# Kernel optimization log

Hardware: AMD Instinct MI355X
Metric: run time of the kernel (lower is better)

Reference implementation:

```python
import jax, jax.numpy as jnp
import numpy as np

NUM_HEADS = 8

def setup_inputs() -> dict:
    key = jax.random.key(0)
    k1, k2, k3, k4, k5 = jax.random.split(key, 5)
    B, N, C = 4, 2048, 512
    x = jax.random.normal(k1, (B, N, C), dtype=jnp.float32)
    s = 1.0 / np.sqrt(C)
    qkv_w = jax.random.uniform(k2, (3 * C, C), dtype=jnp.float32, minval=-s, maxval=s)
    qkv_b = jax.random.uniform(k3, (3 * C,), dtype=jnp.float32, minval=-s, maxval=s)
    proj_w = jax.random.uniform(k4, (C, C), dtype=jnp.float32, minval=-s, maxval=s)
    proj_b = jax.random.uniform(k5, (C,), dtype=jnp.float32, minval=-s, maxval=s)
    return {"x": x, "qkv_w": qkv_w, "qkv_b": qkv_b, "proj_w": proj_w, "proj_b": proj_b}

def reference(x, qkv_w, qkv_b, proj_w, proj_b):
    B, N, C = x.shape
    H = NUM_HEADS
    D = C // H
    scale = D ** -0.5
    # qkv: [B,N,3C] -> [3,B,H,N,D]
    qkv = (jnp.einsum('bnc,oc->bno', x, qkv_w) + qkv_b)
    qkv = qkv.reshape(B, N, 3, H, D).transpose(2, 0, 3, 1, 4)
    q, k, v = qkv[0], qkv[1], qkv[2]
    attn = jnp.einsum('bhnd,bhmd->bhnm', q, k) * scale  # [B,H,N,N]
    attn = jax.nn.softmax(attn, axis=-1)
    out = jnp.einsum('bhnm,bhmd->bhnd', attn, v)  # [B,H,N,D]
    out = out.transpose(0, 2, 1, 3).reshape(B, N, C)
    return jnp.einsum('bnc,oc->bno', out, proj_w) + proj_b
```

## Files before the change

kernel.cpp:

```cpp
#include <hip/hip_runtime.h>
#include <stdint.h>


typedef short bf16x8 __attribute__((ext_vector_type(8)));
typedef float f32x2  __attribute__((ext_vector_type(2)));
typedef float f32x4  __attribute__((ext_vector_type(4)));
typedef float f32x16 __attribute__((ext_vector_type(16)));
typedef unsigned int u32x4 __attribute__((ext_vector_type(4)));

__device__ __forceinline__ unsigned short f2bf(float f) {
    unsigned int u = __builtin_bit_cast(unsigned int, f);
    u += 0x7fffu + ((u >> 16) & 1u);
    return (unsigned short)(u >> 16);
}
__device__ __forceinline__ unsigned int pk2(float a, float b) {
    return (unsigned int)f2bf(a) | ((unsigned int)f2bf(b) << 16);
}
__device__ __forceinline__ float fexp2(float x) {
    return __builtin_amdgcn_exp2f(x);
}
__device__ __forceinline__ bf16x8 ld8_f32(const float* __restrict__ p) {
    float4 f0 = *(const float4*)p;
    float4 f1 = *(const float4*)(p + 4);
    u32x4 u = {pk2(f0.x, f0.y), pk2(f0.z, f0.w), pk2(f1.x, f1.y), pk2(f1.z, f1.w)};
    return __builtin_bit_cast(bf16x8, u);
}
__device__ __forceinline__ void async16(const void* g, void* l) {
    __builtin_amdgcn_global_load_lds(
        (const __attribute__((address_space(1))) unsigned int*)g,
        (__attribute__((address_space(3))) unsigned int*)l,
        16, 0, 0);
}

#define MFMA16(a, b, c) __builtin_amdgcn_mfma_f32_16x16x32_bf16((a), (b), (c), 0, 0, 0)
#define MFMA32(a, b, c) __builtin_amdgcn_mfma_f32_32x32x16_bf16((a), (b), (c), 0, 0, 0)

__global__ void cvt_bf16(const float* __restrict__ x,
                         const float* __restrict__ w,
                         const float* __restrict__ w2,
                         unsigned short* __restrict__ xb,
                         unsigned short* __restrict__ wb,
                         unsigned short* __restrict__ wb2)
{
    const int G = 524288 + 98304 + 32768;
    for (int idx = blockIdx.x * 256 + threadIdx.x; idx < G; idx += gridDim.x * 256) {
        if (idx < 524288)
            *(bf16x8*)(xb + (size_t)idx * 8) = ld8_f32(x + (size_t)idx * 8);
        else if (idx < 524288 + 98304) {
            int j = idx - 524288;
            *(bf16x8*)(wb + (size_t)j * 8) = ld8_f32(w + (size_t)j * 8);
        } else {
            int j = idx - 524288 - 98304;
            *(bf16x8*)(wb2 + (size_t)j * 8) = ld8_f32(w2 + (size_t)j * 8);
        }
    }
}

__global__ __launch_bounds__(256, 4)
void gemm_qkv(const unsigned short* __restrict__ A,
              const unsigned short* __restrict__ B,
              const float* __restrict__ bias,
              unsigned short* __restrict__ out0,
              unsigned short* __restrict__ out1,
              unsigned short* __restrict__ out2,
              int K)
{
    __shared__ unsigned short sA[128 * 32];
    __shared__ unsigned short sB[128 * 32];

    const int tid  = threadIdx.x;
    const int wave = tid >> 6, lane = tid & 63;
    const int l = lane & 15, q16 = lane >> 4;
    const int wm = wave >> 1, wn = wave & 1;
    const int bid = blockIdx.x;
    const int slot = bid >> 3;
    const int m0 = ((bid & 7) * 8 + slot / 12) * 128;
    const int n0 = (slot % 12) * 128;

    f32x4 acc[4][4];
#pragma unroll
    for (int i = 0; i < 4; ++i)
#pragma unroll
        for (int j = 0; j < 4; ++j)
            acc[i][j] = (f32x4){0.f, 0.f, 0.f, 0.f};

    for (int k0 = 0; k0 < K; k0 += 32) {
#pragma unroll
        for (int call = 0; call < 2; ++call) {
            int L = call * 256 + tid;
            int r = L >> 2, c = L & 3;
            async16(A + (size_t)(m0 + r) * K + k0 + c * 8, sA + L * 8);
            async16(B + (size_t)(n0 + r) * K + k0 + c * 8, sB + L * 8);
        }
        __syncthreads();

        bf16x8 af[4], bfr[4];
#pragma unroll
        for (int i = 0; i < 4; ++i)
            af[i] = *(const bf16x8*)(sA + ((wm * 64 + i * 16 + l) * 4 + q16) * 8);
#pragma unroll
        for (int j = 0; j < 4; ++j)
            bfr[j] = *(const bf16x8*)(sB + ((wn * 64 + j * 16 + l) * 4 + q16) * 8);
#pragma unroll
        for (int i = 0; i < 4; ++i)
#pragma unroll
            for (int j = 0; j < 4; ++j)
                acc[i][j] = MFMA16(af[i], bfr[j], acc[i][j]);
        __syncthreads();
    }

    const float lscale = 0.18033688f;
#pragma unroll
    for (int i = 0; i < 4; ++i) {
#pragma unroll
        for (int j = 0; j < 4; ++j) {
            int col = n0 + wn * 64 + j * 16 + l;
            float bv = bias[col];
#pragma unroll
            for (int r = 0; r < 4; ++r) {
                int row = m0 + wm * 64 + i * 16 + q16 * 4 + r;
                float val = acc[i][j][r] + bv;
                int which = col >> 9;
                int hd = (col >> 6) & 7, d = col & 63;
                int b = row >> 11, n = row & 2047;
                int bh = b * 8 + hd;
                if (which == 0) {
                    out0[(size_t)((bh * 2048) + n) * 64 + d] = f2bf(val * lscale);
                } else if (which == 1) {
                    int t = n >> 7, kh2 = (n >> 6) & 1, mt = (n >> 5) & 1;
                    int l31o = n & 31;
                    int ks = (d >> 4) & 3, h2 = (d >> 3) & 1, e = d & 7;
                    size_t frag = ((((size_t)bh * 16 + t) * 2 + kh2) * 2 + mt) * 4 + ks;
                    out1[frag * 512 + (h2 * 32 + l31o) * 8 + e] = f2bf(val);
                } else {
                    int np = (n & ~12) | ((n & 8) >> 1) | ((n & 4) << 1);
                    int t = np >> 7, kh2 = (np >> 6) & 1;
                    int c = (np >> 3) & 7, e = np & 7;
                    int m1 = (c >> 2) & 1, ks2 = (c >> 1) & 1, h2 = c & 1;
                    int dt = d >> 5, l31o = d & 31;
                    size_t frag = (((((size_t)bh * 16 + t) * 2 + kh2) * 2 + m1) * 2
                                   + ks2) * 2 + dt;
                    out2[frag * 512 + (h2 * 32 + l31o) * 8 + e] = f2bf(val);
                }
            }
        }
    }
}

__global__ __launch_bounds__(256, 4)
void gemm_out(const unsigned short* __restrict__ A,
              const unsigned short* __restrict__ B,
              const float* __restrict__ bias,
              float* __restrict__ outf,
              int K, int N)
{
    __shared__ unsigned short sA[64 * 32];
    __shared__ unsigned short sB[128 * 32];

    const int tid  = threadIdx.x;
    const int wave = tid >> 6, lane = tid & 63;
    const int l = lane & 15, q16 = lane >> 4;
    const int wm = wave >> 1, wn = wave & 1;
    const int bid = blockIdx.x;
    const int slot = bid >> 3;
    const int m0 = ((bid & 7) * 16 + (slot >> 2)) * 64;
    const int n0 = (slot & 3) * 128;

    f32x4 acc[2][4];
#pragma unroll
    for (int i = 0; i < 2; ++i)
#pragma unroll
        for (int j = 0; j < 4; ++j)
            acc[i][j] = (f32x4){0.f, 0.f, 0.f, 0.f};

    for (int k0 = 0; k0 < K; k0 += 32) {
        {
            int r = tid >> 2, c = tid & 3;
            async16(A + (size_t)(m0 + r) * K + k0 + c * 8, sA + tid * 8);
        }
#pragma unroll
        for (int call = 0; call < 2; ++call) {
            int L = call * 256 + tid;
            int r = L >> 2, c = L & 3;
            async16(B + (size_t)(n0 + r) * K + k0 + c * 8, sB + L * 8);
        }
        __syncthreads();

        bf16x8 af[2], bfr[4];
#pragma unroll
        for (int i = 0; i < 2; ++i)
            af[i] = *(const bf16x8*)(sA + ((wm * 32 + i * 16 + l) * 4 + q16) * 8);
#pragma unroll
        for (int j = 0; j < 4; ++j)
            bfr[j] = *(const bf16x8*)(sB + ((wn * 64 + j * 16 + l) * 4 + q16) * 8);
#pragma unroll
        for (int i = 0; i < 2; ++i)
#pragma unroll
            for (int j = 0; j < 4; ++j)
                acc[i][j] = MFMA16(af[i], bfr[j], acc[i][j]);
        __syncthreads();
    }

#pragma unroll
    for (int i = 0; i < 2; ++i) {
#pragma unroll
        for (int j = 0; j < 4; ++j) {
            int col = n0 + wn * 64 + j * 16 + l;
            float bv = bias[col];
#pragma unroll
            for (int r = 0; r < 4; ++r) {
                int row = m0 + wm * 32 + i * 16 + q16 * 4 + r;
                outf[(size_t)row * N + col] = acc[i][j][r] + bv;
            }
        }
    }
}

__global__ __launch_bounds__(512)
void attn_fused(const unsigned short* __restrict__ Q,
                const unsigned short* __restrict__ Kfr,
                const unsigned short* __restrict__ Vfr,
                unsigned short* __restrict__ O)
{
    __shared__ float smrg[16384 + 1024];

    const int tid  = threadIdx.x;
    const int wave = tid >> 6, lane = tid & 63;
    const int l31 = lane & 31, h = lane >> 5;
    const int qq = wave & 3, kh = wave >> 2;
    const int bid = blockIdx.x;
    const int slot = bid >> 3;
    const int bh = (bid & 7) * 4 + (slot >> 3);
    const int qc = slot & 7;
    const int q0 = qc * 256 + qq * 64;

    const unsigned short* Kb = Kfr + (size_t)bh * 131072 + kh * 4096 + lane * 8;
    const unsigned short* Vb = Vfr + (size_t)bh * 131072 + kh * 4096 + lane * 8;

    bf16x8 qf[2][4];
#pragma unroll
    for (int qt = 0; qt < 2; ++qt)
#pragma unroll
        for (int ks = 0; ks < 4; ++ks)
            qf[qt][ks] = *(const bf16x8*)(Q + (size_t)(bh * 2048 + q0 + qt * 32 + l31) * 64
                                          + ks * 16 + h * 8);

    f32x16 oacc[2][2];
#pragma unroll
    for (int qt = 0; qt < 2; ++qt)
#pragma unroll
        for (int dt = 0; dt < 2; ++dt)
#pragma unroll
            for (int e = 0; e < 16; ++e) oacc[qt][dt][e] = 0.f;
    f32x16 Zv;
#pragma unroll
    for (int e = 0; e < 16; ++e) Zv[e] = 0.f;
    f32x2 l2[2];
    l2[0] = (f32x2){0.f, 0.f};
    l2[1] = (f32x2){0.f, 0.f};

    auto softmax_pack = [&](const f32x16& s0, const f32x16& s1,
                            bf16x8& f00, bf16x8& f01,
                            bf16x8& f10, bf16x8& f11) {
        unsigned int pk0[4][2], pk1[4][2];
#pragma unroll
        for (int g = 0; g < 4; ++g) {
            float a0 = fexp2(s0[4 * g + 0]);
            float a1 = fexp2(s0[4 * g + 1]);
            float a2 = fexp2(s0[4 * g + 2]);
            float a3 = fexp2(s0[4 * g + 3]);
            l2[0] += (f32x2){a0, a1};
            l2[0] += (f32x2){a2, a3};
            pk0[g][0] = __builtin_amdgcn_perm(
                __builtin_bit_cast(unsigned int, a1),
                __builtin_bit_cast(unsigned int, a0), 0x07060302u);
            pk0[g][1] = __builtin_amdgcn_perm(
                __builtin_bit_cast(unsigned int, a3),
                __builtin_bit_cast(unsigned int, a2), 0x07060302u);
            float b0 = fexp2(s1[4 * g + 0]);
            float b1 = fexp2(s1[4 * g + 1]);
            float b2 = fexp2(s1[4 * g + 2]);
            float b3 = fexp2(s1[4 * g + 3]);
            l2[1] += (f32x2){b0, b1};
            l2[1] += (f32x2){b2, b3};
            pk1[g][0] = __builtin_amdgcn_perm(
                __builtin_bit_cast(unsigned int, b1),
                __builtin_bit_cast(unsigned int, b0), 0x07060302u);
            pk1[g][1] = __builtin_amdgcn_perm(
                __builtin_bit_cast(unsigned int, b3),
                __builtin_bit_cast(unsigned int, b2), 0x07060302u);
        }
        u32x4 bu;
        bu[0] = pk0[0][0]; bu[1] = pk0[0][1]; bu[2] = pk0[1][0]; bu[3] = pk0[1][1];
        f00 = __builtin_bit_cast(bf16x8, bu);
        bu[0] = pk0[2][0]; bu[1] = pk0[2][1]; bu[2] = pk0[3][0]; bu[3] = pk0[3][1];
        f01 = __builtin_bit_cast(bf16x8, bu);
        bu[0] = pk1[0][0]; bu[1] = pk1[0][1]; bu[2] = pk1[1][0]; bu[3] = pk1[1][1];
        f10 = __builtin_bit_cast(bf16x8, bu);
        bu[0] = pk1[2][0]; bu[1] = pk1[2][1]; bu[2] = pk1[3][0]; bu[3] = pk1[3][1];
        f11 = __builtin_bit_cast(bf16x8, bu);
    };

    bf16x8 kA[4], kB[4], vv[2][2];

#pragma unroll
    for (int ks = 0; ks < 4; ++ks)
        kA[ks] = *(const bf16x8*)(Kb + ks * 512);

    for (int t = 0; t < 16; ++t) {
        const size_t tb = (size_t)t * 8192;

#pragma unroll
        for (int ks2 = 0; ks2 < 2; ++ks2)
#pragma unroll
            for (int dt = 0; dt < 2; ++dt)
                vv[ks2][dt] = *(const bf16x8*)(Vb + tb + ks2 * 1024 + dt * 512);
#pragma unroll
        for (int ks = 0; ks < 4; ++ks)
            kB[ks] = *(const bf16x8*)(Kb + tb + 2048 + ks * 512);

        f32x16 s0, s1;
        __builtin_amdgcn_s_setprio(1);
        s0 = MFMA32(kA[0], qf[0][0], Zv);
        s1 = MFMA32(kA[0], qf[1][0], Zv);
#pragma unroll
        for (int ks = 1; ks < 4; ++ks) {
            s0 = MFMA32(kA[ks], qf[0][ks], s0);
            s1 = MFMA32(kA[ks], qf[1][ks], s1);
        }
        __builtin_amdgcn_s_setprio(0);
        {
            bf16x8 f00, f01, f10, f11;
            softmax_pack(s0, s1, f00, f01, f10, f11);
            __builtin_amdgcn_s_setprio(1);
            oacc[0][0] = MFMA32(vv[0][0], f00, oacc[0][0]);
            oacc[1][0] = MFMA32(vv[0][0], f10, oacc[1][0]);
            oacc[0][1] = MFMA32(vv[0][1], f00, oacc[0][1]);
            oacc[1][1] = MFMA32(vv[0][1], f10, oacc[1][1]);
            oacc[0][0] = MFMA32(vv[1][0], f01, oacc[0][0]);
            oacc[1][0] = MFMA32(vv[1][0], f11, oacc[1][0]);
            oacc[0][1] = MFMA32(vv[1][1], f01, oacc[0][1]);
            oacc[1][1] = MFMA32(vv[1][1], f11, oacc[1][1]);
            __builtin_amdgcn_s_setprio(0);
        }

#pragma unroll
        for (int ks2 = 0; ks2 < 2; ++ks2)
#pragma unroll
            for (int dt = 0; dt < 2; ++dt)
                vv[ks2][dt] = *(const bf16x8*)(Vb + tb + 2048 + ks2 * 1024 + dt * 512);
        if (t < 15) {
#pragma unroll
            for (int ks = 0; ks < 4; ++ks)
                kA[ks] = *(const bf16x8*)(Kb + tb + 8192 + ks * 512);
        }

        __builtin_amdgcn_s_setprio(1);
        s0 = MFMA32(kB[0], qf[0][0], Zv);
        s1 = MFMA32(kB[0], qf[1][0], Zv);
#pragma unroll
        for (int ks = 1; ks < 4; ++ks) {
            s0 = MFMA32(kB[ks], qf[0][ks], s0);
            s1 = MFMA32(kB[ks], qf[1][ks], s1);
        }
        __builtin_amdgcn_s_setprio(0);
        {
            bf16x8 f00, f01, f10, f11;
            softmax_pack(s0, s1, f00, f01, f10, f11);
            __builtin_amdgcn_s_setprio(1);
            oacc[0][0] = MFMA32(vv[0][0], f00, oacc[0][0]);
            oacc[1][0] = MFMA32(vv[0][0], f10, oacc[1][0]);
            oacc[0][1] = MFMA32(vv[0][1], f00, oacc[0][1]);
            oacc[1][1] = MFMA32(vv[0][1], f10, oacc[1][1]);
            oacc[0][0] = MFMA32(vv[1][0], f01, oacc[0][0]);
            oacc[1][0] = MFMA32(vv[1][0], f11, oacc[1][0]);
            oacc[0][1] = MFMA32(vv[1][1], f01, oacc[0][1]);
            oacc[1][1] = MFMA32(vv[1][1], f11, oacc[1][1]);
            __builtin_amdgcn_s_setprio(0);
        }
    }

    __syncthreads();
    float* sf = smrg;
    float* sl = smrg + 16384;
    if (kh == 1) {
        const int base = (qq * 64 + lane) * 64;
#pragma unroll
        for (int qt = 0; qt < 2; ++qt)
#pragma unroll
            for (int dt = 0; dt < 2; ++dt) {
                int chunk = (qt * 2 + dt) ^ (lane & 3);
                *(f32x16*)(sf + base + chunk * 16) = oacc[qt][dt];
            }
        *(f32x2*)(sl + (qq * 64 + lane) * 4 + 0) = l2[0];
        *(f32x2*)(sl + (qq * 64 + lane) * 4 + 2) = l2[1];
    }
    __syncthreads();
    if (kh == 0) {
        const int base = (qq * 64 + lane) * 64;
#pragma unroll
        for (int qt = 0; qt < 2; ++qt)
#pragma unroll
            for (int dt = 0; dt < 2; ++dt) {
                int chunk = (qt * 2 + dt) ^ (lane & 3);
                f32x16 part = *(const f32x16*)(sf + base + chunk * 16);
#pragma unroll
                for (int e = 0; e < 16; ++e) oacc[qt][dt][e] += part[e];
            }
        l2[0] += *(const f32x2*)(sl + (qq * 64 + lane) * 4 + 0);
        l2[1] += *(const f32x2*)(sl + (qq * 64 + lane) * 4 + 2);

        const int b = bh >> 3, hh = bh & 7;
#pragma unroll
        for (int qt = 0; qt < 2; ++qt) {
            float l_run = l2[qt][0] + l2[qt][1];
            l_run += __shfl_xor(l_run, 32);
            float inv = 1.f / fmaxf(l_run, 1e-20f);
            unsigned short* obase = O + ((size_t)(b * 2048 + q0 + qt * 32 + l31)) * 512 + hh * 64;
#pragma unroll
            for (int dt = 0; dt < 2; ++dt)
#pragma unroll
                for (int g = 0; g < 4; ++g) {
                    int d = dt * 32 + 8 * g + 4 * h;
                    unsigned int w0 = pk2(oacc[qt][dt][4 * g + 0] * inv,
                                          oacc[qt][dt][4 * g + 1] * inv);
                    unsigned int w1 = pk2(oacc[qt][dt][4 * g + 2] * inv,
                                          oacc[qt][dt][4 * g + 3] * inv);
                    uint2 w = {w0, w1};
                    *(uint2*)(obase + d) = w;
                }
        }
    }
}

extern "C" void kernel_launch(void* const* d_in, const int* in_sizes, int n_in,
                              void* d_out, int out_size, void* d_ws, size_t ws_size,
                              hipStream_t stream)
{
    const float* x      = (const float*)d_in[0];
    const float* qkv_w  = (const float*)d_in[1];
    const float* qkv_b  = (const float*)d_in[2];
    const float* proj_w = (const float*)d_in[3];
    const float* proj_b = (const float*)d_in[4];

    const size_t PER = 4u * 8u * 2048u * 64u;
    unsigned short* q_ws  = (unsigned short*)d_ws;
    unsigned short* k_ws  = q_ws  + PER;
    unsigned short* vt_ws = k_ws  + PER;
    unsigned short* ao_ws = vt_ws + PER;
    unsigned short* wb2   = ao_ws + PER;

    unsigned short* xb = (unsigned short*)d_out;
    unsigned short* wb = xb + PER;

    cvt_bf16<<<dim3(640), 256, 0, stream>>>(x, qkv_w, proj_w, xb, wb, wb2);
    gemm_qkv<<<dim3(768), 256, 0, stream>>>(xb, wb, qkv_b, q_ws, k_ws, vt_ws, 512);
    attn_fused<<<dim3(256), 512, 0, stream>>>(q_ws, k_ws, vt_ws, ao_ws);
    gemm_out<<<dim3(512), 256, 0, stream>>>(ao_ws, wb2, proj_b, (float*)d_out, 512, 512);
}
```

Before: 151.6 us.

## Split attention keys four ways per block and double grid to 512 blocks

Each attention block now covers 128 queries with 2 query waves by 4 key-split waves, instead of 256 queries with 4 by 2, and the grid doubles to 512 blocks. Partial outputs and row sums are merged with a two-level shared-memory tree reduction. The manual double-buffered K/V register prefetch is dropped for a simpler per-tile load, and the launch bounds now request 3 waves per SIMD. This aims to give more blocks for the CUs and more latency hiding through occupancy, at the cost of extra reduction passes and barriers and of reloading Q per block.

```diff
diff --git a/kernel.cpp b/kernel.cpp
--- a/kernel.cpp
+++ b/kernel.cpp
@@ -216,7 +216,7 @@
     }
 }
 
-__global__ __launch_bounds__(512)
+__global__ __launch_bounds__(512, 3)
 void attn_fused(const unsigned short* __restrict__ Q,
                 const unsigned short* __restrict__ Kfr,
                 const unsigned short* __restrict__ Vfr,
@@ -227,15 +227,15 @@
     const int tid  = threadIdx.x;
     const int wave = tid >> 6, lane = tid & 63;
     const int l31 = lane & 31, h = lane >> 5;
-    const int qq = wave & 3, kh = wave >> 2;
+    const int qq = wave & 1, kq = wave >> 1;
     const int bid = blockIdx.x;
     const int slot = bid >> 3;
-    const int bh = (bid & 7) * 4 + (slot >> 3);
-    const int qc = slot & 7;
-    const int q0 = qc * 256 + qq * 64;
-
-    const unsigned short* Kb = Kfr + (size_t)bh * 131072 + kh * 4096 + lane * 8;
-    const unsigned short* Vb = Vfr + (size_t)bh * 131072 + kh * 4096 + lane * 8;
+    const int bh = (bid & 7) * 4 + (slot >> 4);
+    const int qc = slot & 15;
+    const int q0 = qc * 128 + qq * 64;
+
+    const unsigned short* Kb = Kfr + (size_t)bh * 131072 + kq * 2048 + lane * 8;
+    const unsigned short* Vb = Vfr + (size_t)bh * 131072 + kq * 2048 + lane * 8;
 
     bf16x8 qf[2][4];
 #pragma unroll
@@ -259,9 +259,30 @@
     l2[0] = (f32x2){0.f, 0.f};
     l2[1] = (f32x2){0.f, 0.f};
 
-    auto softmax_pack = [&](const f32x16& s0, const f32x16& s1,
-                            bf16x8& f00, bf16x8& f01,
-                            bf16x8& f10, bf16x8& f11) {
+    for (int t = 0; t < 16; ++t) {
+        const size_t tb = (size_t)t * 8192;
+
+        bf16x8 k0 = *(const bf16x8*)(Kb + tb + 0 * 512);
+        bf16x8 k1 = *(const bf16x8*)(Kb + tb + 1 * 512);
+        bf16x8 k2 = *(const bf16x8*)(Kb + tb + 2 * 512);
+        bf16x8 k3 = *(const bf16x8*)(Kb + tb + 3 * 512);
+        bf16x8 v00 = *(const bf16x8*)(Vb + tb + 0 * 1024 + 0 * 512);
+        bf16x8 v01 = *(const bf16x8*)(Vb + tb + 0 * 1024 + 1 * 512);
+        bf16x8 v10 = *(const bf16x8*)(Vb + tb + 1 * 1024 + 0 * 512);
+        bf16x8 v11 = *(const bf16x8*)(Vb + tb + 1 * 1024 + 1 * 512);
+
+        f32x16 s0, s1;
+        __builtin_amdgcn_s_setprio(1);
+        s0 = MFMA32(k0, qf[0][0], Zv);
+        s1 = MFMA32(k0, qf[1][0], Zv);
+        s0 = MFMA32(k1, qf[0][1], s0);
+        s1 = MFMA32(k1, qf[1][1], s1);
+        s0 = MFMA32(k2, qf[0][2], s0);
+        s1 = MFMA32(k2, qf[1][2], s1);
+        s0 = MFMA32(k3, qf[0][3], s0);
+        s1 = MFMA32(k3, qf[1][3], s1);
+        __builtin_amdgcn_s_setprio(0);
+
         unsigned int pk0[4][2], pk1[4][2];
 #pragma unroll
         for (int g = 0; g < 4; ++g) {
@@ -292,99 +313,33 @@
         }
         u32x4 bu;
         bu[0] = pk0[0][0]; bu[1] = pk0[0][1]; bu[2] = pk0[1][0]; bu[3] = pk0[1][1];
-        f00 = __builtin_bit_cast(bf16x8, bu);
+        bf16x8 f00 = __builtin_bit_cast(bf16x8, bu);
         bu[0] = pk0[2][0]; bu[1] = pk0[2][1]; bu[2] = pk0[3][0]; bu[3] = pk0[3][1];
-        f01 = __builtin_bit_cast(bf16x8, bu);
+        bf16x8 f01 = __builtin_bit_cast(bf16x8, bu);
         bu[0] = pk1[0][0]; bu[1] = pk1[0][1]; bu[2] = pk1[1][0]; bu[3] = pk1[1][1];
-        f10 = __builtin_bit_cast(bf16x8, bu);
+        bf16x8 f10 = __builtin_bit_cast(bf16x8, bu);
         bu[0] = pk1[2][0]; bu[1] = pk1[2][1]; bu[2] = pk1[3][0]; bu[3] = pk1[3][1];
-        f11 = __builtin_bit_cast(bf16x8, bu);
-    };
-
-    bf16x8 kA[4], kB[4], vv[2][2];
-
-#pragma unroll
-    for (int ks = 0; ks < 4; ++ks)
-        kA[ks] = *(const bf16x8*)(Kb + ks * 512);
-
-    for (int t = 0; t < 16; ++t) {
-        const size_t tb = (size_t)t * 8192;
-
-#pragma unroll
-        for (int ks2 = 0; ks2 < 2; ++ks2)
-#pragma unroll
-            for (int dt = 0; dt < 2; ++dt)
-                vv[ks2][dt] = *(const bf16x8*)(Vb + tb + ks2 * 1024 + dt * 512);
-#pragma unroll
-        for (int ks = 0; ks < 4; ++ks)
-            kB[ks] = *(const bf16x8*)(Kb + tb + 2048 + ks * 512);
-
-        f32x16 s0, s1;
+        bf16x8 f11 = __builtin_bit_cast(bf16x8, bu);
+
         __builtin_amdgcn_s_setprio(1);
-        s0 = MFMA32(kA[0], qf[0][0], Zv);
-        s1 = MFMA32(kA[0], qf[1][0], Zv);
-#pragma unroll
-        for (int ks = 1; ks < 4; ++ks) {
-            s0 = MFMA32(kA[ks], qf[0][ks], s0);
-            s1 = MFMA32(kA[ks], qf[1][ks], s1);
-        }
+        oacc[0][0] = MFMA32(v00, f00, oacc[0][0]);
+        oacc[1][0] = MFMA32(v00, f10, oacc[1][0]);
+        oacc[0][1] = MFMA32(v01, f00, oacc[0][1]);
+        oacc[1][1] = MFMA32(v01, f10, oacc[1][1]);
+        oacc[0][0] = MFMA32(v10, f01, oacc[0][0]);
+        oacc[1][0] = MFMA32(v10, f11, oacc[1][0]);
+        oacc[0][1] = MFMA32(v11, f01, oacc[0][1]);
+        oacc[1][1] = MFMA32(v11, f11, oacc[1][1]);
         __builtin_amdgcn_s_setprio(0);
-        {
-            bf16x8 f00, f01, f10, f11;
-            softmax_pack(s0, s1, f00, f01, f10, f11);
-            __builtin_amdgcn_s_setprio(1);
-            oacc[0][0] = MFMA32(vv[0][0], f00, oacc[0][0]);
-            oacc[1][0] = MFMA32(vv[0][0], f10, oacc[1][0]);
-            oacc[0][1] = MFMA32(vv[0][1], f00, oacc[0][1]);
-            oacc[1][1] = MFMA32(vv[0][1], f10, oacc[1][1]);
-            oacc[0][0] = MFMA32(vv[1][0], f01, oacc[0][0]);
-            oacc[1][0] = MFMA32(vv[1][0], f11, oacc[1][0]);
-            oacc[0][1] = MFMA32(vv[1][1], f01, oacc[0][1]);
-            oacc[1][1] = MFMA32(vv[1][1], f11, oacc[1][1]);
-            __builtin_amdgcn_s_setprio(0);
-        }
-
-#pragma unroll
-        for (int ks2 = 0; ks2 < 2; ++ks2)
-#pragma unroll
-            for (int dt = 0; dt < 2; ++dt)
-                vv[ks2][dt] = *(const bf16x8*)(Vb + tb + 2048 + ks2 * 1024 + dt * 512);
-        if (t < 15) {
-#pragma unroll
-            for (int ks = 0; ks < 4; ++ks)
-                kA[ks] = *(const bf16x8*)(Kb + tb + 8192 + ks * 512);
-        }
-
-        __builtin_amdgcn_s_setprio(1);
-        s0 = MFMA32(kB[0], qf[0][0], Zv);
-        s1 = MFMA32(kB[0], qf[1][0], Zv);
-#pragma unroll
-        for (int ks = 1; ks < 4; ++ks) {
-            s0 = MFMA32(kB[ks], qf[0][ks], s0);
-            s1 = MFMA32(kB[ks], qf[1][ks], s1);
-        }
-        __builtin_amdgcn_s_setprio(0);
-        {
-            bf16x8 f00, f01, f10, f11;
-            softmax_pack(s0, s1, f00, f01, f10, f11);
-            __builtin_amdgcn_s_setprio(1);
-            oacc[0][0] = MFMA32(vv[0][0], f00, oacc[0][0]);
-            oacc[1][0] = MFMA32(vv[0][0], f10, oacc[1][0]);
-            oacc[0][1] = MFMA32(vv[0][1], f00, oacc[0][1]);
-            oacc[1][1] = MFMA32(vv[0][1], f10, oacc[1][1]);
-            oacc[0][0] = MFMA32(vv[1][0], f01, oacc[0][0]);
-            oacc[1][0] = MFMA32(vv[1][0], f11, oacc[1][0]);
-            oacc[0][1] = MFMA32(vv[1][1], f01, oacc[0][1]);
-            oacc[1][1] = MFMA32(vv[1][1], f11, oacc[1][1]);
-            __builtin_amdgcn_s_setprio(0);
-        }
-    }
-
-    __syncthreads();
+    }
+
     float* sf = smrg;
     float* sl = smrg + 16384;
-    if (kh == 1) {
-        const int base = (qq * 64 + lane) * 64;
+
+    __syncthreads();
+    if (kq & 1) {
+        const int s = kq >> 1;
+        const int base = ((qq * 2 + s) * 64 + lane) * 64;
 #pragma unroll
         for (int qt = 0; qt < 2; ++qt)
 #pragma unroll
@@ -392,11 +347,41 @@
                 int chunk = (qt * 2 + dt) ^ (lane & 3);
                 *(f32x16*)(sf + base + chunk * 16) = oacc[qt][dt];
             }
+        *(f32x2*)(sl + ((qq * 2 + s) * 64 + lane) * 4 + 0) = l2[0];
+        *(f32x2*)(sl + ((qq * 2 + s) * 64 + lane) * 4 + 2) = l2[1];
+    }
+    __syncthreads();
+    if (!(kq & 1)) {
+        const int s = kq >> 1;
+        const int base = ((qq * 2 + s) * 64 + lane) * 64;
+#pragma unroll
+        for (int qt = 0; qt < 2; ++qt)
+#pragma unroll
+            for (int dt = 0; dt < 2; ++dt) {
+                int chunk = (qt * 2 + dt) ^ (lane & 3);
+                f32x16 part = *(const f32x16*)(sf + base + chunk * 16);
+#pragma unroll
+                for (int e = 0; e < 16; ++e) oacc[qt][dt][e] += part[e];
+            }
+        l2[0] += *(const f32x2*)(sl + ((qq * 2 + s) * 64 + lane) * 4 + 0);
+        l2[1] += *(const f32x2*)(sl + ((qq * 2 + s) * 64 + lane) * 4 + 2);
+    }
+
+    __syncthreads();
+    if (kq == 2) {
+        const int base = (qq * 64 + lane) * 64;
+#pragma unroll
+        for (int qt = 0; qt < 2; ++qt)
+#pragma unroll
+            for (int dt = 0; dt < 2; ++dt) {
+                int chunk = (qt * 2 + dt) ^ (lane & 3);
+                *(f32x16*)(sf + base + chunk * 16) = oacc[qt][dt];
+            }
         *(f32x2*)(sl + (qq * 64 + lane) * 4 + 0) = l2[0];
         *(f32x2*)(sl + (qq * 64 + lane) * 4 + 2) = l2[1];
     }
     __syncthreads();
-    if (kh == 0) {
+    if (kq == 0) {
         const int base = (qq * 64 + lane) * 64;
 #pragma unroll
         for (int qt = 0; qt < 2; ++qt)
@@ -455,6 +440,6 @@
 
     cvt_bf16<<<dim3(640), 256, 0, stream>>>(x, qkv_w, proj_w, xb, wb, wb2);
     gemm_qkv<<<dim3(768), 256, 0, stream>>>(xb, wb, qkv_b, q_ws, k_ws, vt_ws, 512);
-    attn_fused<<<dim3(256), 512, 0, stream>>>(q_ws, k_ws, vt_ws, ao_ws);
+    attn_fused<<<dim3(512), 512, 0, stream>>>(q_ws, k_ws, vt_ws, ao_ws);
     gemm_out<<<dim3(512), 256, 0, stream>>>(ao_ws, wb2, proj_b, (float*)d_out, 512, 512);
 }
```

New measurement: 157.2 us. 1.04x slower.
